# Kernel optimization log

Measured on AMD Instinct MI355X. Metric: run time of the kernel, lower is better.

## Reference

```python
import jax, jax.numpy as jnp
import numpy as np

SEQ_LEN, BATCH, IN_SIZE = 512, 1024, 3
HID, HID_FC, OUT = 512, 512, 1
HORIZON = 96


def gru_cell(x, h, w_ih, w_hh, b_ih, b_hh):
    # PyTorch GRU cell math. x: [B, in], h: [B, H], w_ih: [3H, in], w_hh: [3H, H]
    gi = x @ w_ih.T + b_ih
    gh = h @ w_hh.T + b_hh
    i_r, i_z, i_n = jnp.split(gi, 3, axis=-1)
    h_r, h_z, h_n = jnp.split(gh, 3, axis=-1)
    r = jax.nn.sigmoid(i_r + h_r)
    z = jax.nn.sigmoid(i_z + h_z)
    n = jnp.tanh(i_n + r * h_n)
    return (1.0 - z) * n + z * h


def setup_inputs() -> dict:
    key = jax.random.key(0)
    ks = jax.random.split(key, 16)
    s_in = 1.0 / np.sqrt(HID)
    inp = {
        'src': jax.random.normal(ks[0], (SEQ_LEN, BATCH, IN_SIZE), dtype=jnp.float32),
        'enc_wih': jax.random.uniform(ks[1], (3 * HID, IN_SIZE), minval=-s_in, maxval=s_in),
        'enc_whh': jax.random.uniform(ks[2], (3 * HID, HID), minval=-s_in, maxval=s_in),
        'enc_bih': jax.random.uniform(ks[3], (3 * HID,), minval=-s_in, maxval=s_in),
        'enc_bhh': jax.random.uniform(ks[4], (3 * HID,), minval=-s_in, maxval=s_in),
        'dec_wih': jax.random.uniform(ks[5], (3 * HID, OUT), minval=-s_in, maxval=s_in),
        'dec_whh': jax.random.uniform(ks[6], (3 * HID, HID), minval=-s_in, maxval=s_in),
        'dec_bih': jax.random.uniform(ks[7], (3 * HID,), minval=-s_in, maxval=s_in),
        'dec_bhh': jax.random.uniform(ks[8], (3 * HID,), minval=-s_in, maxval=s_in),
        'w1': jax.random.uniform(ks[9], (HID_FC, HID), minval=-s_in, maxval=s_in),
        'b1': jax.random.uniform(ks[10], (HID_FC,), minval=-s_in, maxval=s_in),
        'w2': jax.random.uniform(ks[11], (OUT, HID_FC), minval=-1.0 / np.sqrt(HID_FC), maxval=1.0 / np.sqrt(HID_FC)),
        'b2': jax.random.uniform(ks[12], (OUT,), minval=-1.0 / np.sqrt(HID_FC), maxval=1.0 / np.sqrt(HID_FC)),
        'horizon': HORIZON,
    }
    return inp


def reference(src, enc_wih, enc_whh, enc_bih, enc_bhh,
              dec_wih, dec_whh, dec_bih, dec_bhh,
              w1, b1, w2, b2, horizon):
    B = src.shape[1]
    h0 = jnp.zeros((B, HID), dtype=src.dtype)

    # Encoder: run GRU over time; only final hidden state is used.
    def enc_step(h, x_t):
        return gru_cell(x_t, h, enc_wih, enc_whh, enc_bih, enc_bhh), None
    h, _ = jax.lax.scan(enc_step, h0, src)

    dec_in0 = src[-1, :, 0:1]  # [B, 1]

    def dec_step(carry, _):
        dec_in, h = carry
        h = gru_cell(dec_in, h, dec_wih, dec_whh, dec_bih, dec_bhh)
        y = jax.nn.relu(h @ w1.T + b1) @ w2.T + b2  # [B, 1]
        return (y, h), y
    _, outputs = jax.lax.scan(dec_step, (dec_in0, h), None, length=horizon)
    return outputs  # [horizon, B, 1]
```

## Files before the change

kernel.cpp:

```cpp
#include <hip/hip_runtime.h>

typedef __bf16 bf16x8 __attribute__((ext_vector_type(8)));
typedef float f32x4 __attribute__((ext_vector_type(4)));

#define HID 512
#define BATCH 1024
#define SEQL 512
#define NWG 512
#define NTHR 256

#define OFF_ENH 0u
#define OFF_ENL 1572864u
#define OFF_DEH 3145728u
#define OFF_DEL 4718592u
#define OFF_W1H 6291456u
#define OFF_W1L 6815744u
#define OFF_HP0 7340032u
#define OFF_HP1 9437184u
#define OFF_FC1 11534336u
#define OFF_BAR 13631488u
#define WS_NEED 13639680u

#define LDS_LO 16384
#define SWZ(row, cb) (((row) << 10) + ((cb) ^ (((row) & 7) << 4)))

__device__ __forceinline__ f32x4 mfma16(bf16x8 a, bf16x8 b, f32x4 c) {
  return __builtin_amdgcn_mfma_f32_16x16x32_bf16(a, b, c, 0, 0, 0);
}
__device__ __forceinline__ float sig_(float x) { return 1.0f / (1.0f + __expf(-x)); }
__device__ __forceinline__ float tanh_(float x) { return 1.0f - 2.0f / (__expf(2.0f * x) + 1.0f); }

__device__ __forceinline__ unsigned long long ald64(const void* p) {
  return __hip_atomic_load((const unsigned long long*)p, __ATOMIC_RELAXED,
                           __HIP_MEMORY_SCOPE_AGENT);
}
__device__ __forceinline__ void ast32(void* p, unsigned v) {
  __hip_atomic_store((unsigned*)p, v, __ATOMIC_RELAXED, __HIP_MEMORY_SCOPE_AGENT);
}
__device__ __forceinline__ void astf(void* p, float v) {
  __hip_atomic_store((float*)p, v, __ATOMIC_RELAXED, __HIP_MEMORY_SCOPE_AGENT);
}

__global__ void split_w(const float* __restrict__ a, __bf16* __restrict__ hi,
                        __bf16* __restrict__ lo, int n) {
  int i = blockIdx.x * blockDim.x + threadIdx.x;
  if (i < n) {
    float v = a[i];
    __bf16 h = (__bf16)v;
    hi[i] = h;
    lo[i] = (__bf16)(v - (float)h);
  }
}

__device__ __forceinline__ void gbar(unsigned* cnt, unsigned target) {
  __syncthreads();
  if (threadIdx.x == 0) {
    __hip_atomic_fetch_add(cnt, 1u, __ATOMIC_RELAXED, __HIP_MEMORY_SCOPE_AGENT);
    int i = 0;
    while (__hip_atomic_load(cnt, __ATOMIC_RELAXED, __HIP_MEMORY_SCOPE_AGENT) < target) {
      __builtin_amdgcn_s_sleep(2);
      if (++i >= 30000) break;
    }
  }
  __syncthreads();
  __builtin_amdgcn_sched_barrier(0);
}

__device__ __forceinline__ void stage_h16(char* sm, const unsigned* hsrc, int row0, int tid) {
  const unsigned long long* src = (const unsigned long long*)hsrc + ((size_t)row0 << 8) + tid;
  unsigned long long b[16];
#pragma unroll
  for (int j = 0; j < 16; ++j) b[j] = ald64(src + (size_t)j * 256);
#pragma unroll
  for (int j = 0; j < 16; ++j) {
    const unsigned p0 = (unsigned)b[j];
    const unsigned p1 = (unsigned)(b[j] >> 32);
    const unsigned hw = (p0 & 0xffffu) | (p1 << 16);
    const unsigned lw = (p0 >> 16) | (p1 & 0xffff0000u);
    const int sa = SWZ(j, tid << 2);
    *(unsigned*)(sm + sa) = hw;
    *(unsigned*)(sm + LDS_LO + sa) = lw;
  }
}

__device__ __forceinline__ void gh3(const char* sm, int rl, int kbb,
                                    const __bf16* __restrict__ Bh,
                                    const __bf16* __restrict__ Bl,
                                    const int (&boff)[3], f32x4 (&acc)[3]) {
#pragma unroll 4
  for (int kc = 0; kc < 16; ++kc) {
    const int sa = SWZ(rl, (kc << 6) + kbb);
    bf16x8 ah = *(const bf16x8*)(sm + sa);
    bf16x8 al = *(const bf16x8*)(sm + LDS_LO + sa);
    const int ko = kc << 5;
#pragma unroll
    for (int f = 0; f < 3; ++f) {
      bf16x8 bh = *(const bf16x8*)(Bh + boff[f] + ko);
      bf16x8 bl = *(const bf16x8*)(Bl + boff[f] + ko);
      acc[f] = mfma16(ah, bh, acc[f]);
      acc[f] = mfma16(al, bh, acc[f]);
      acc[f] = mfma16(ah, bl, acc[f]);
    }
  }
}

__device__ __forceinline__ void gh1(const char* sm, int rl, int kbb,
                                    const __bf16* __restrict__ Bh,
                                    const __bf16* __restrict__ Bl, int boff, f32x4& acc) {
#pragma unroll 4
  for (int kc = 0; kc < 16; ++kc) {
    const int sa = SWZ(rl, (kc << 6) + kbb);
    bf16x8 ah = *(const bf16x8*)(sm + sa);
    bf16x8 al = *(const bf16x8*)(sm + LDS_LO + sa);
    const int ko = kc << 5;
    bf16x8 bh = *(const bf16x8*)(Bh + boff + ko);
    bf16x8 bl = *(const bf16x8*)(Bl + boff + ko);
    acc = mfma16(ah, bh, acc);
    acc = mfma16(al, bh, acc);
    acc = mfma16(ah, bl, acc);
  }
}

__global__ void __launch_bounds__(NTHR, 4) seq2seq_main(
    const float* __restrict__ src, const float* __restrict__ enc_wih,
    const float* __restrict__ enc_bih, const float* __restrict__ enc_bhh,
    const float* __restrict__ dec_wih, const float* __restrict__ dec_bih,
    const float* __restrict__ dec_bhh, const float* __restrict__ b1,
    const float* __restrict__ w2, const float* __restrict__ b2,
    const int* __restrict__ hor, float* __restrict__ out, char* __restrict__ ws) {
  __shared__ f32x4 smv[2048];
  char* sm = (char*)smv;
  float* yb = (float*)sm;

  const __bf16* ench_hi = (const __bf16*)(ws + OFF_ENH);
  const __bf16* ench_lo = (const __bf16*)(ws + OFF_ENL);
  const __bf16* dech_hi = (const __bf16*)(ws + OFF_DEH);
  const __bf16* dech_lo = (const __bf16*)(ws + OFF_DEL);
  const __bf16* w1h = (const __bf16*)(ws + OFF_W1H);
  const __bf16* w1l = (const __bf16*)(ws + OFF_W1L);
  unsigned* hp0 = (unsigned*)(ws + OFF_HP0);
  unsigned* hp1 = (unsigned*)(ws + OFF_HP1);
  float* fc1 = (float*)(ws + OFF_FC1);

  const int bid = blockIdx.x;
  const int G = bid >> 3;
  const int ct = bid & 7;
  const int tid = threadIdx.x;
  const int wv = tid >> 6;
  const int lane = tid & 63;
  const int lan15 = lane & 15;
  const int crow = (lane >> 4) << 2;
  const int kbe = (lane >> 4) << 3;
  const int kbb = kbe << 1;
  const int rl = lan15;
  const int row0 = G << 4;
  const int cg = (ct << 6) + (wv << 4) + lan15;

  unsigned* cnt = (unsigned*)(ws + OFF_BAR) + (G << 5);

  int boff[3];
#pragma unroll
  for (int g = 0; g < 3; ++g) boff[g] = ((g << 9) + cg) * HID + kbe;
  const int boff_fc = cg * HID + kbe;

  float wE[3][3], biE[3], bhE[3];
#pragma unroll
  for (int g = 0; g < 3; ++g) {
    const int j = (g << 9) + cg;
    wE[g][0] = enc_wih[j * 3 + 0];
    wE[g][1] = enc_wih[j * 3 + 1];
    wE[g][2] = enc_wih[j * 3 + 2];
    biE[g] = enc_bih[j];
    bhE[g] = enc_bhh[j];
  }

  const f32x4 zf = {0.0f, 0.0f, 0.0f, 0.0f};
  float hpv[4] = {0.f, 0.f, 0.f, 0.f};

  for (int t = 0; t < SEQL; ++t) {
    float xv[4][3];
#pragma unroll
    for (int reg = 0; reg < 4; ++reg) {
      const int row = row0 + crow + reg;
      const float* xp = src + ((size_t)t * BATCH + row) * 3;
      xv[reg][0] = xp[0];
      xv[reg][1] = xp[1];
      xv[reg][2] = xp[2];
    }

    f32x4 acc[3];
#pragma unroll
    for (int f = 0; f < 3; ++f) acc[f] = zf;

    if (t != 0) {
      stage_h16(sm, (t & 1) ? hp1 : hp0, row0, tid);
      __syncthreads();
      gh3(sm, rl, kbb, ench_hi, ench_lo, boff, acc);
    }

    unsigned* hn = ((t + 1) & 1) ? hp1 : hp0;
#pragma unroll
    for (int reg = 0; reg < 4; ++reg) {
      const int row = row0 + crow + reg;
      const float x0 = xv[reg][0], x1 = xv[reg][1], x2 = xv[reg][2];
      const float gir = fmaf(x0, wE[0][0], fmaf(x1, wE[0][1], fmaf(x2, wE[0][2], biE[0])));
      const float giz = fmaf(x0, wE[1][0], fmaf(x1, wE[1][1], fmaf(x2, wE[1][2], biE[1])));
      const float gin = fmaf(x0, wE[2][0], fmaf(x1, wE[2][1], fmaf(x2, wE[2][2], biE[2])));
      const float rg = sig_(gir + acc[0][reg] + bhE[0]);
      const float zg = sig_(giz + acc[1][reg] + bhE[1]);
      const float ng = tanh_(gin + rg * (acc[2][reg] + bhE[2]));
      const float hv = fmaf(zg, hpv[reg] - ng, ng);
      hpv[reg] = hv;
      const __bf16 hb = (__bf16)hv;
      const __bf16 lb = (__bf16)(hv - (float)hb);
      const unsigned pw = (unsigned)__builtin_bit_cast(unsigned short, hb) |
                          ((unsigned)__builtin_bit_cast(unsigned short, lb) << 16);
      ast32(hn + (size_t)row * HID + cg, pw);
    }
    gbar(cnt, 8u * (unsigned)(t + 1));
  }

  float wD[3], biD[3], bhD[3];
#pragma unroll
  for (int g = 0; g < 3; ++g) {
    const int j = (g << 9) + cg;
    wD[g] = dec_wih[j];
    biD[g] = dec_bih[j];
    bhD[g] = dec_bhh[j];
  }
  const float b1c = b1[cg];
  const float b2v = b2[0];
  float w2p0[4], w2p1[4];
#pragma unroll
  for (int j = 0; j < 4; ++j) {
    w2p0[j] = w2[2 * (lane + j * 64)];
    w2p1[j] = w2[2 * (lane + j * 64) + 1];
  }
  int H = hor[0];
  if (H < 1 || H > 96) H = 96;

  for (int t = 0; t < H; ++t) {
    float din[4];
    if (t == 0) {
#pragma unroll
      for (int reg = 0; reg < 4; ++reg) {
        const int row = row0 + crow + reg;
        din[reg] = src[((size_t)(SEQL - 1) * BATCH + row) * 3];
      }
    } else {
#pragma unroll
      for (int rr = 0; rr < 4; ++rr) {
        const int row = row0 + (wv << 2) + rr;
        const unsigned long long* fp = (const unsigned long long*)fc1 + ((size_t)row << 8);
        float s = 0.0f;
#pragma unroll
        for (int j = 0; j < 4; ++j) {
          const unsigned long long w = ald64(fp + lane + (j << 6));
          const float f0 = __builtin_bit_cast(float, (unsigned)(w & 0xffffffffULL));
          const float f1 = __builtin_bit_cast(float, (unsigned)(w >> 32));
          s = fmaf(f0, w2p0[j], fmaf(f1, w2p1[j], s));
        }
#pragma unroll
        for (int off = 1; off < 64; off <<= 1) s += __shfl_xor(s, off, 64);
        if (lane == 0) yb[(wv << 2) + rr] = s + b2v;
      }
      __syncthreads();
      if (ct == 0 && tid < 16) out[(size_t)(t - 1) * BATCH + row0 + tid] = yb[tid];
#pragma unroll
      for (int reg = 0; reg < 4; ++reg) din[reg] = yb[crow + reg];
      __syncthreads();
    }

    {
      stage_h16(sm, (t & 1) ? hp1 : hp0, row0, tid);
      __syncthreads();
      f32x4 acc[3];
#pragma unroll
      for (int f = 0; f < 3; ++f) acc[f] = zf;
      gh3(sm, rl, kbb, dech_hi, dech_lo, boff, acc);

      unsigned* hn = ((t + 1) & 1) ? hp1 : hp0;
#pragma unroll
      for (int reg = 0; reg < 4; ++reg) {
        const int row = row0 + crow + reg;
        const float d = din[reg];
        const float rg = sig_(fmaf(d, wD[0], biD[0]) + acc[0][reg] + bhD[0]);
        const float zg = sig_(fmaf(d, wD[1], biD[1]) + acc[1][reg] + bhD[1]);
        const float ng = tanh_(fmaf(d, wD[2], biD[2]) + rg * (acc[2][reg] + bhD[2]));
        const float hv = fmaf(zg, hpv[reg] - ng, ng);
        hpv[reg] = hv;
        const __bf16 hb = (__bf16)hv;
        const __bf16 lb = (__bf16)(hv - (float)hb);
        const unsigned pw = (unsigned)__builtin_bit_cast(unsigned short, hb) |
                            ((unsigned)__builtin_bit_cast(unsigned short, lb) << 16);
        ast32(hn + (size_t)row * HID + cg, pw);
      }
    }
    gbar(cnt, 8u * (unsigned)(SEQL + 2 * t + 1));

    {
      stage_h16(sm, ((t + 1) & 1) ? hp1 : hp0, row0, tid);
      __syncthreads();
      f32x4 fa = zf;
      gh1(sm, rl, kbb, w1h, w1l, boff_fc, fa);
#pragma unroll
      for (int reg = 0; reg < 4; ++reg) {
        const int row = row0 + crow + reg;
        astf(&fc1[(size_t)row * HID + cg], fmaxf(fa[reg] + b1c, 0.0f));
      }
    }
    gbar(cnt, 8u * (unsigned)(SEQL + 2 * t + 2));
  }

  if (ct == 0) {
#pragma unroll
    for (int rr = 0; rr < 4; ++rr) {
      const int row = row0 + (wv << 2) + rr;
      const unsigned long long* fp = (const unsigned long long*)fc1 + ((size_t)row << 8);
      float s = 0.0f;
#pragma unroll
      for (int j = 0; j < 4; ++j) {
        const unsigned long long w = ald64(fp + lane + (j << 6));
        const float f0 = __builtin_bit_cast(float, (unsigned)(w & 0xffffffffULL));
        const float f1 = __builtin_bit_cast(float, (unsigned)(w >> 32));
        s = fmaf(f0, w2p0[j], fmaf(f1, w2p1[j], s));
      }
#pragma unroll
      for (int off = 1; off < 64; off <<= 1) s += __shfl_xor(s, off, 64);
      if (lane == 0) yb[(wv << 2) + rr] = s + b2v;
    }
    __syncthreads();
    if (tid < 16) out[(size_t)(H - 1) * BATCH + row0 + tid] = yb[tid];
  }
}

extern "C" void kernel_launch(void* const* d_in, const int* in_sizes, int n_in,
                              void* d_out, int out_size, void* d_ws, size_t ws_size,
                              hipStream_t stream) {
  if (ws_size < WS_NEED) return;

  const float* src = (const float*)d_in[0];
  const float* enc_wih = (const float*)d_in[1];
  const float* enc_whh = (const float*)d_in[2];
  const float* enc_bih = (const float*)d_in[3];
  const float* enc_bhh = (const float*)d_in[4];
  const float* dec_wih = (const float*)d_in[5];
  const float* dec_whh = (const float*)d_in[6];
  const float* dec_bih = (const float*)d_in[7];
  const float* dec_bhh = (const float*)d_in[8];
  const float* w1 = (const float*)d_in[9];
  const float* b1 = (const float*)d_in[10];
  const float* w2 = (const float*)d_in[11];
  const float* b2 = (const float*)d_in[12];
  const int* hor = (const int*)d_in[13];
  float* out = (float*)d_out;
  char* ws = (char*)d_ws;

  hipMemsetAsync(ws + OFF_BAR, 0, 8192, stream);

  split_w<<<dim3(3072), dim3(256), 0, stream>>>(enc_whh, (__bf16*)(ws + OFF_ENH),
                                                (__bf16*)(ws + OFF_ENL), 786432);
  split_w<<<dim3(3072), dim3(256), 0, stream>>>(dec_whh, (__bf16*)(ws + OFF_DEH),
                                                (__bf16*)(ws + OFF_DEL), 786432);
  split_w<<<dim3(1024), dim3(256), 0, stream>>>(w1, (__bf16*)(ws + OFF_W1H),
                                                (__bf16*)(ws + OFF_W1L), 262144);

  seq2seq_main<<<dim3(NWG), dim3(NTHR), 0, stream>>>(
      src, enc_wih, enc_bih, enc_bhh, dec_wih, dec_bih, dec_bhh, b1, w2, b2, hor, out, ws);
}
```

Baseline: 15.33 ms.

## Give each workgroup a full batch tile and keep hidden state in LDS

The work split changes from 512 workgroups (8 column tiles per 16-row batch group, tied together by global-memory barriers) to 64 workgroups of 512 threads. Each workgroup now owns all 512 hidden columns for its 16 batch rows. Hidden state stays in LDS, so the global h exchange, the atomic spin barriers and the fc1 round trip through memory go away, and the FC2 reduction is done in LDS. The trade-off is that only 64 workgroups run on a GPU with many more CUs, and each one streams the full recurrent weights from cache every step, so far less of the chip is used.

New measurement: 55.52 ms. +262.3%, slower.

```diff
diff --git a/kernel.cpp b/kernel.cpp
--- a/kernel.cpp
+++ b/kernel.cpp
@@ -2,12 +2,13 @@
 
 typedef __bf16 bf16x8 __attribute__((ext_vector_type(8)));
 typedef float f32x4 __attribute__((ext_vector_type(4)));
+typedef unsigned u32x4 __attribute__((ext_vector_type(4)));
 
 #define HID 512
 #define BATCH 1024
 #define SEQL 512
-#define NWG 512
-#define NTHR 256
+#define NWG 64
+#define NTHR 512
 
 #define OFF_ENH 0u
 #define OFF_ENL 1572864u
@@ -15,31 +16,17 @@
 #define OFF_DEL 4718592u
 #define OFF_W1H 6291456u
 #define OFF_W1L 6815744u
-#define OFF_HP0 7340032u
-#define OFF_HP1 9437184u
-#define OFF_FC1 11534336u
-#define OFF_BAR 13631488u
-#define WS_NEED 13639680u
-
-#define LDS_LO 16384
-#define SWZ(row, cb) (((row) << 10) + ((cb) ^ (((row) & 7) << 4)))
+#define WS_NEED 7340032u
+
+#define LDS_PS 32768
+#define LDS_Y 33280
+#define SWZP(row, cb) (((row) << 11) + ((cb) ^ (((row) & 7) << 4)))
 
 __device__ __forceinline__ f32x4 mfma16(bf16x8 a, bf16x8 b, f32x4 c) {
   return __builtin_amdgcn_mfma_f32_16x16x32_bf16(a, b, c, 0, 0, 0);
 }
 __device__ __forceinline__ float sig_(float x) { return 1.0f / (1.0f + __expf(-x)); }
 __device__ __forceinline__ float tanh_(float x) { return 1.0f - 2.0f / (__expf(2.0f * x) + 1.0f); }
-
-__device__ __forceinline__ unsigned long long ald64(const void* p) {
-  return __hip_atomic_load((const unsigned long long*)p, __ATOMIC_RELAXED,
-                           __HIP_MEMORY_SCOPE_AGENT);
-}
-__device__ __forceinline__ void ast32(void* p, unsigned v) {
-  __hip_atomic_store((unsigned*)p, v, __ATOMIC_RELAXED, __HIP_MEMORY_SCOPE_AGENT);
-}
-__device__ __forceinline__ void astf(void* p, float v) {
-  __hip_atomic_store((float*)p, v, __ATOMIC_RELAXED, __HIP_MEMORY_SCOPE_AGENT);
-}
 
 __global__ void split_w(const float* __restrict__ a, __bf16* __restrict__ hi,
                         __bf16* __restrict__ lo, int n) {
@@ -52,85 +39,34 @@
   }
 }
 
-__device__ __forceinline__ void gbar(unsigned* cnt, unsigned target) {
-  __syncthreads();
-  if (threadIdx.x == 0) {
-    __hip_atomic_fetch_add(cnt, 1u, __ATOMIC_RELAXED, __HIP_MEMORY_SCOPE_AGENT);
-    int i = 0;
-    while (__hip_atomic_load(cnt, __ATOMIC_RELAXED, __HIP_MEMORY_SCOPE_AGENT) < target) {
-      __builtin_amdgcn_s_sleep(2);
-      if (++i >= 30000) break;
-    }
-  }
-  __syncthreads();
-  __builtin_amdgcn_sched_barrier(0);
-}
-
-__device__ __forceinline__ void stage_h16(char* sm, const unsigned* hsrc, int row0, int tid) {
-  const unsigned long long* src = (const unsigned long long*)hsrc + ((size_t)row0 << 8) + tid;
-  unsigned long long b[16];
-#pragma unroll
-  for (int j = 0; j < 16; ++j) b[j] = ald64(src + (size_t)j * 256);
-#pragma unroll
-  for (int j = 0; j < 16; ++j) {
-    const unsigned p0 = (unsigned)b[j];
-    const unsigned p1 = (unsigned)(b[j] >> 32);
-    const unsigned hw = (p0 & 0xffffu) | (p1 << 16);
-    const unsigned lw = (p0 >> 16) | (p1 & 0xffff0000u);
-    const int sa = SWZ(j, tid << 2);
-    *(unsigned*)(sm + sa) = hw;
-    *(unsigned*)(sm + LDS_LO + sa) = lw;
-  }
-}
-
-__device__ __forceinline__ void gh3(const char* sm, int rl, int kbb,
-                                    const __bf16* __restrict__ Bh,
-                                    const __bf16* __restrict__ Bl,
-                                    const int (&boff)[3], f32x4 (&acc)[3]) {
-#pragma unroll 4
-  for (int kc = 0; kc < 16; ++kc) {
-    const int sa = SWZ(rl, (kc << 6) + kbb);
-    bf16x8 ah = *(const bf16x8*)(sm + sa);
-    bf16x8 al = *(const bf16x8*)(sm + LDS_LO + sa);
-    const int ko = kc << 5;
-#pragma unroll
-    for (int f = 0; f < 3; ++f) {
-      bf16x8 bh = *(const bf16x8*)(Bh + boff[f] + ko);
-      bf16x8 bl = *(const bf16x8*)(Bl + boff[f] + ko);
-      acc[f] = mfma16(ah, bh, acc[f]);
-      acc[f] = mfma16(al, bh, acc[f]);
-      acc[f] = mfma16(ah, bl, acc[f]);
-    }
-  }
-}
-
-__device__ __forceinline__ void gh1(const char* sm, int rl, int kbb,
-                                    const __bf16* __restrict__ Bh,
-                                    const __bf16* __restrict__ Bl, int boff, f32x4& acc) {
-#pragma unroll 4
-  for (int kc = 0; kc < 16; ++kc) {
-    const int sa = SWZ(rl, (kc << 6) + kbb);
-    bf16x8 ah = *(const bf16x8*)(sm + sa);
-    bf16x8 al = *(const bf16x8*)(sm + LDS_LO + sa);
-    const int ko = kc << 5;
-    bf16x8 bh = *(const bf16x8*)(Bh + boff + ko);
-    bf16x8 bl = *(const bf16x8*)(Bl + boff + ko);
-    acc = mfma16(ah, bh, acc);
-    acc = mfma16(al, bh, acc);
-    acc = mfma16(ah, bl, acc);
-  }
-}
-
-__global__ void __launch_bounds__(NTHR, 4) seq2seq_main(
+__device__ __forceinline__ void rd_afrag(const char* sm, int lan15, int cb, bf16x8& ah,
+                                         bf16x8& al) {
+  const u32x4 q0 = *(const u32x4*)(sm + SWZP(lan15, cb));
+  const u32x4 q1 = *(const u32x4*)(sm + SWZP(lan15, cb + 16));
+  u32x4 h, l;
+  h.x = (q0.x & 0xffffu) | (q0.y << 16);
+  h.y = (q0.z & 0xffffu) | (q0.w << 16);
+  h.z = (q1.x & 0xffffu) | (q1.y << 16);
+  h.w = (q1.z & 0xffffu) | (q1.w << 16);
+  l.x = (q0.x >> 16) | (q0.y & 0xffff0000u);
+  l.y = (q0.z >> 16) | (q0.w & 0xffff0000u);
+  l.z = (q1.x >> 16) | (q1.y & 0xffff0000u);
+  l.w = (q1.z >> 16) | (q1.w & 0xffff0000u);
+  ah = __builtin_bit_cast(bf16x8, h);
+  al = __builtin_bit_cast(bf16x8, l);
+}
+
+__global__ void __launch_bounds__(NTHR, 2) seq2seq_main(
     const float* __restrict__ src, const float* __restrict__ enc_wih,
     const float* __restrict__ enc_bih, const float* __restrict__ enc_bhh,
     const float* __restrict__ dec_wih, const float* __restrict__ dec_bih,
     const float* __restrict__ dec_bhh, const float* __restrict__ b1,
     const float* __restrict__ w2, const float* __restrict__ b2,
     const int* __restrict__ hor, float* __restrict__ out, char* __restrict__ ws) {
-  __shared__ f32x4 smv[2048];
+  __shared__ f32x4 smv[2084];
   char* sm = (char*)smv;
-  float* yb = (float*)sm;
+  float* psum = (float*)(sm + LDS_PS);
+  float* ylds = (float*)(sm + LDS_Y);
 
   const __bf16* ench_hi = (const __bf16*)(ws + OFF_ENH);
   const __bf16* ench_lo = (const __bf16*)(ws + OFF_ENL);
@@ -138,199 +74,256 @@
   const __bf16* dech_lo = (const __bf16*)(ws + OFF_DEL);
   const __bf16* w1h = (const __bf16*)(ws + OFF_W1H);
   const __bf16* w1l = (const __bf16*)(ws + OFF_W1L);
-  unsigned* hp0 = (unsigned*)(ws + OFF_HP0);
-  unsigned* hp1 = (unsigned*)(ws + OFF_HP1);
-  float* fc1 = (float*)(ws + OFF_FC1);
-
-  const int bid = blockIdx.x;
-  const int G = bid >> 3;
-  const int ct = bid & 7;
+
+  const int G = blockIdx.x;
+  const int row0 = G << 4;
   const int tid = threadIdx.x;
   const int wv = tid >> 6;
   const int lane = tid & 63;
   const int lan15 = lane & 15;
-  const int crow = (lane >> 4) << 2;
-  const int kbe = (lane >> 4) << 3;
-  const int kbb = kbe << 1;
-  const int rl = lan15;
-  const int row0 = G << 4;
-  const int cg = (ct << 6) + (wv << 4) + lan15;
-
-  unsigned* cnt = (unsigned*)(ws + OFF_BAR) + (G << 5);
-
-  int boff[3];
-#pragma unroll
-  for (int g = 0; g < 3; ++g) boff[g] = ((g << 9) + cg) * HID + kbe;
-  const int boff_fc = cg * HID + kbe;
-
-  float wE[3][3], biE[3], bhE[3];
-#pragma unroll
-  for (int g = 0; g < 3; ++g) {
-    const int j = (g << 9) + cg;
-    wE[g][0] = enc_wih[j * 3 + 0];
-    wE[g][1] = enc_wih[j * 3 + 1];
-    wE[g][2] = enc_wih[j * 3 + 2];
-    biE[g] = enc_bih[j];
-    bhE[g] = enc_bhh[j];
-  }
+  const int l4 = lane >> 4;
+  const int kbe = l4 << 3;
+
+  int boff[3][4];
+#pragma unroll
+  for (int g = 0; g < 3; ++g)
+#pragma unroll
+    for (int nf = 0; nf < 4; ++nf)
+      boff[g][nf] = (((g << 9) + (wv << 6) + (nf << 4) + lan15) << 9) + kbe;
+  int bofffc[4];
+#pragma unroll
+  for (int nf = 0; nf < 4; ++nf) bofffc[nf] = (((wv << 6) + (nf << 4) + lan15) << 9) + kbe;
+
+  float wE[3][4][3], biE[3][4], bhE[3][4];
+#pragma unroll
+  for (int g = 0; g < 3; ++g)
+#pragma unroll
+    for (int nf = 0; nf < 4; ++nf) {
+      const int j = (g << 9) + (wv << 6) + (nf << 4) + lan15;
+      wE[g][nf][0] = enc_wih[j * 3 + 0];
+      wE[g][nf][1] = enc_wih[j * 3 + 1];
+      wE[g][nf][2] = enc_wih[j * 3 + 2];
+      biE[g][nf] = enc_bih[j];
+      bhE[g][nf] = enc_bhh[j];
+    }
 
   const f32x4 zf = {0.0f, 0.0f, 0.0f, 0.0f};
-  float hpv[4] = {0.f, 0.f, 0.f, 0.f};
+  float hpv[4][4];
+#pragma unroll
+  for (int nf = 0; nf < 4; ++nf)
+#pragma unroll
+    for (int reg = 0; reg < 4; ++reg) hpv[nf][reg] = 0.0f;
 
   for (int t = 0; t < SEQL; ++t) {
     float xv[4][3];
 #pragma unroll
     for (int reg = 0; reg < 4; ++reg) {
-      const int row = row0 + crow + reg;
-      const float* xp = src + ((size_t)t * BATCH + row) * 3;
+      const int grow = row0 + (l4 << 2) + reg;
+      const float* xp = src + ((size_t)t * BATCH + grow) * 3;
       xv[reg][0] = xp[0];
       xv[reg][1] = xp[1];
       xv[reg][2] = xp[2];
     }
 
-    f32x4 acc[3];
-#pragma unroll
-    for (int f = 0; f < 3; ++f) acc[f] = zf;
+    f32x4 acc[3][4];
+#pragma unroll
+    for (int g = 0; g < 3; ++g)
+#pragma unroll
+      for (int nf = 0; nf < 4; ++nf) acc[g][nf] = zf;
 
     if (t != 0) {
-      stage_h16(sm, (t & 1) ? hp1 : hp0, row0, tid);
-      __syncthreads();
-      gh3(sm, rl, kbb, ench_hi, ench_lo, boff, acc);
-    }
-
-    unsigned* hn = ((t + 1) & 1) ? hp1 : hp0;
+#pragma unroll 4
+      for (int kc = 0; kc < 16; ++kc) {
+        bf16x8 ah, al;
+        rd_afrag(sm, lan15, (kc << 7) + (l4 << 5), ah, al);
+        const int ko = kc << 5;
+#pragma unroll
+        for (int g = 0; g < 3; ++g)
+#pragma unroll
+          for (int nf = 0; nf < 4; ++nf) {
+            bf16x8 bh = *(const bf16x8*)(ench_hi + boff[g][nf] + ko);
+            bf16x8 bl = *(const bf16x8*)(ench_lo + boff[g][nf] + ko);
+            acc[g][nf] = mfma16(ah, bh, acc[g][nf]);
+            acc[g][nf] = mfma16(al, bh, acc[g][nf]);
+            acc[g][nf] = mfma16(ah, bl, acc[g][nf]);
+          }
+      }
+    }
+    __syncthreads();
+
 #pragma unroll
     for (int reg = 0; reg < 4; ++reg) {
-      const int row = row0 + crow + reg;
+      const int row = (l4 << 2) + reg;
       const float x0 = xv[reg][0], x1 = xv[reg][1], x2 = xv[reg][2];
-      const float gir = fmaf(x0, wE[0][0], fmaf(x1, wE[0][1], fmaf(x2, wE[0][2], biE[0])));
-      const float giz = fmaf(x0, wE[1][0], fmaf(x1, wE[1][1], fmaf(x2, wE[1][2], biE[1])));
-      const float gin = fmaf(x0, wE[2][0], fmaf(x1, wE[2][1], fmaf(x2, wE[2][2], biE[2])));
-      const float rg = sig_(gir + acc[0][reg] + bhE[0]);
-      const float zg = sig_(giz + acc[1][reg] + bhE[1]);
-      const float ng = tanh_(gin + rg * (acc[2][reg] + bhE[2]));
-      const float hv = fmaf(zg, hpv[reg] - ng, ng);
-      hpv[reg] = hv;
-      const __bf16 hb = (__bf16)hv;
-      const __bf16 lb = (__bf16)(hv - (float)hb);
-      const unsigned pw = (unsigned)__builtin_bit_cast(unsigned short, hb) |
-                          ((unsigned)__builtin_bit_cast(unsigned short, lb) << 16);
-      ast32(hn + (size_t)row * HID + cg, pw);
-    }
-    gbar(cnt, 8u * (unsigned)(t + 1));
-  }
-
-  float wD[3], biD[3], bhD[3];
-#pragma unroll
-  for (int g = 0; g < 3; ++g) {
-    const int j = (g << 9) + cg;
-    wD[g] = dec_wih[j];
-    biD[g] = dec_bih[j];
-    bhD[g] = dec_bhh[j];
-  }
-  const float b1c = b1[cg];
-  const float b2v = b2[0];
-  float w2p0[4], w2p1[4];
-#pragma unroll
-  for (int j = 0; j < 4; ++j) {
-    w2p0[j] = w2[2 * (lane + j * 64)];
-    w2p1[j] = w2[2 * (lane + j * 64) + 1];
-  }
-  int H = hor[0];
-  if (H < 1 || H > 96) H = 96;
-
-  for (int t = 0; t < H; ++t) {
-    float din[4];
-    if (t == 0) {
-#pragma unroll
-      for (int reg = 0; reg < 4; ++reg) {
-        const int row = row0 + crow + reg;
-        din[reg] = src[((size_t)(SEQL - 1) * BATCH + row) * 3];
-      }
-    } else {
-#pragma unroll
-      for (int rr = 0; rr < 4; ++rr) {
-        const int row = row0 + (wv << 2) + rr;
-        const unsigned long long* fp = (const unsigned long long*)fc1 + ((size_t)row << 8);
-        float s = 0.0f;
-#pragma unroll
-        for (int j = 0; j < 4; ++j) {
-          const unsigned long long w = ald64(fp + lane + (j << 6));
-          const float f0 = __builtin_bit_cast(float, (unsigned)(w & 0xffffffffULL));
-          const float f1 = __builtin_bit_cast(float, (unsigned)(w >> 32));
-          s = fmaf(f0, w2p0[j], fmaf(f1, w2p1[j], s));
-        }
-#pragma unroll
-        for (int off = 1; off < 64; off <<= 1) s += __shfl_xor(s, off, 64);
-        if (lane == 0) yb[(wv << 2) + rr] = s + b2v;
-      }
-      __syncthreads();
-      if (ct == 0 && tid < 16) out[(size_t)(t - 1) * BATCH + row0 + tid] = yb[tid];
-#pragma unroll
-      for (int reg = 0; reg < 4; ++reg) din[reg] = yb[crow + reg];
-      __syncthreads();
-    }
-
-    {
-      stage_h16(sm, (t & 1) ? hp1 : hp0, row0, tid);
-      __syncthreads();
-      f32x4 acc[3];
-#pragma unroll
-      for (int f = 0; f < 3; ++f) acc[f] = zf;
-      gh3(sm, rl, kbb, dech_hi, dech_lo, boff, acc);
-
-      unsigned* hn = ((t + 1) & 1) ? hp1 : hp0;
-#pragma unroll
-      for (int reg = 0; reg < 4; ++reg) {
-        const int row = row0 + crow + reg;
-        const float d = din[reg];
-        const float rg = sig_(fmaf(d, wD[0], biD[0]) + acc[0][reg] + bhD[0]);
-        const float zg = sig_(fmaf(d, wD[1], biD[1]) + acc[1][reg] + bhD[1]);
-        const float ng = tanh_(fmaf(d, wD[2], biD[2]) + rg * (acc[2][reg] + bhD[2]));
-        const float hv = fmaf(zg, hpv[reg] - ng, ng);
-        hpv[reg] = hv;
+#pragma unroll
+      for (int nf = 0; nf < 4; ++nf) {
+        const float gir =
+            fmaf(x0, wE[0][nf][0], fmaf(x1, wE[0][nf][1], fmaf(x2, wE[0][nf][2], biE[0][nf])));
+        const float giz =
+            fmaf(x0, wE[1][nf][0], fmaf(x1, wE[1][nf][1], fmaf(x2, wE[1][nf][2], biE[1][nf])));
+        const float gin =
+            fmaf(x0, wE[2][nf][0], fmaf(x1, wE[2][nf][1], fmaf(x2, wE[2][nf][2], biE[2][nf])));
+        const float rg = sig_(gir + acc[0][nf][reg] + bhE[0][nf]);
+        const float zg = sig_(giz + acc[1][nf][reg] + bhE[1][nf]);
+        const float ng = tanh_(gin + rg * (acc[2][nf][reg] + bhE[2][nf]));
+        const float hv = fmaf(zg, hpv[nf][reg] - ng, ng);
+        hpv[nf][reg] = hv;
         const __bf16 hb = (__bf16)hv;
         const __bf16 lb = (__bf16)(hv - (float)hb);
         const unsigned pw = (unsigned)__builtin_bit_cast(unsigned short, hb) |
                             ((unsigned)__builtin_bit_cast(unsigned short, lb) << 16);
-        ast32(hn + (size_t)row * HID + cg, pw);
-      }
-    }
-    gbar(cnt, 8u * (unsigned)(SEQL + 2 * t + 1));
-
-    {
-      stage_h16(sm, ((t + 1) & 1) ? hp1 : hp0, row0, tid);
+        const int col = (wv << 6) + (nf << 4) + lan15;
+        *(unsigned*)(sm + SWZP(row, col << 2)) = pw;
+      }
+    }
+    __syncthreads();
+  }
+
+  float wD[3][4], biD[3][4], bhD[3][4], b1c[4], w2v[4];
+#pragma unroll
+  for (int g = 0; g < 3; ++g)
+#pragma unroll
+    for (int nf = 0; nf < 4; ++nf) {
+      const int j = (g << 9) + (wv << 6) + (nf << 4) + lan15;
+      wD[g][nf] = dec_wih[j];
+      biD[g][nf] = dec_bih[j];
+      bhD[g][nf] = dec_bhh[j];
+    }
+#pragma unroll
+  for (int nf = 0; nf < 4; ++nf) {
+    const int fcol = (wv << 6) + (nf << 4) + lan15;
+    b1c[nf] = b1[fcol];
+    w2v[nf] = w2[fcol];
+  }
+  const float b2v = b2[0];
+  int H = hor[0];
+  if (H < 1 || H > 96) H = 96;
+
+  float facc[4][4];
+
+  for (int t = 0; t < H; ++t) {
+    float din[4];
+    if (t == 0) {
+#pragma unroll
+      for (int reg = 0; reg < 4; ++reg)
+        din[reg] = src[((size_t)(SEQL - 1) * BATCH + row0 + (l4 << 2) + reg) * 3];
+    } else {
+      float ps[4];
+#pragma unroll
+      for (int reg = 0; reg < 4; ++reg) {
+        ps[reg] = facc[0][reg] * w2v[0];
+#pragma unroll
+        for (int nf = 1; nf < 4; ++nf) ps[reg] = fmaf(facc[nf][reg], w2v[nf], ps[reg]);
+#pragma unroll
+        for (int off = 1; off < 16; off <<= 1) ps[reg] += __shfl_xor(ps[reg], off, 64);
+      }
+      if (lan15 == 0) {
+#pragma unroll
+        for (int reg = 0; reg < 4; ++reg) psum[(((l4 << 2) + reg) << 3) + wv] = ps[reg];
+      }
       __syncthreads();
-      f32x4 fa = zf;
-      gh1(sm, rl, kbb, w1h, w1l, boff_fc, fa);
-#pragma unroll
-      for (int reg = 0; reg < 4; ++reg) {
-        const int row = row0 + crow + reg;
-        astf(&fc1[(size_t)row * HID + cg], fmaxf(fa[reg] + b1c, 0.0f));
-      }
-    }
-    gbar(cnt, 8u * (unsigned)(SEQL + 2 * t + 2));
-  }
-
-  if (ct == 0) {
-#pragma unroll
-    for (int rr = 0; rr < 4; ++rr) {
-      const int row = row0 + (wv << 2) + rr;
-      const unsigned long long* fp = (const unsigned long long*)fc1 + ((size_t)row << 8);
-      float s = 0.0f;
-#pragma unroll
-      for (int j = 0; j < 4; ++j) {
-        const unsigned long long w = ald64(fp + lane + (j << 6));
-        const float f0 = __builtin_bit_cast(float, (unsigned)(w & 0xffffffffULL));
-        const float f1 = __builtin_bit_cast(float, (unsigned)(w >> 32));
-        s = fmaf(f0, w2p0[j], fmaf(f1, w2p1[j], s));
-      }
-#pragma unroll
-      for (int off = 1; off < 64; off <<= 1) s += __shfl_xor(s, off, 64);
-      if (lane == 0) yb[(wv << 2) + rr] = s + b2v;
-    }
-    __syncthreads();
-    if (tid < 16) out[(size_t)(H - 1) * BATCH + row0 + tid] = yb[tid];
+      if (wv == 0 && lane < 16) {
+        float s = b2v;
+#pragma unroll
+        for (int j = 0; j < 8; ++j) s += psum[(lane << 3) + j];
+        ylds[lane] = s;
+        out[(size_t)(t - 1) * BATCH + row0 + lane] = s;
+      }
+      __syncthreads();
+#pragma unroll
+      for (int reg = 0; reg < 4; ++reg) din[reg] = ylds[(l4 << 2) + reg];
+    }
+
+    f32x4 acc[3][4];
+#pragma unroll
+    for (int g = 0; g < 3; ++g)
+#pragma unroll
+      for (int nf = 0; nf < 4; ++nf) acc[g][nf] = zf;
+#pragma unroll 4
+    for (int kc = 0; kc < 16; ++kc) {
+      bf16x8 ah, al;
+      rd_afrag(sm, lan15, (kc << 7) + (l4 << 5), ah, al);
+      const int ko = kc << 5;
+#pragma unroll
+      for (int g = 0; g < 3; ++g)
+#pragma unroll
+        for (int nf = 0; nf < 4; ++nf) {
+          bf16x8 bh = *(const bf16x8*)(dech_hi + boff[g][nf] + ko);
+          bf16x8 bl = *(const bf16x8*)(dech_lo + boff[g][nf] + ko);
+          acc[g][nf] = mfma16(ah, bh, acc[g][nf]);
+          acc[g][nf] = mfma16(al, bh, acc[g][nf]);
+          acc[g][nf] = mfma16(ah, bl, acc[g][nf]);
+        }
+    }
+    __syncthreads();
+
+#pragma unroll
+    for (int reg = 0; reg < 4; ++reg) {
+      const int row = (l4 << 2) + reg;
+      const float d = din[reg];
+#pragma unroll
+      for (int nf = 0; nf < 4; ++nf) {
+        const float rg = sig_(fmaf(d, wD[0][nf], biD[0][nf]) + acc[0][nf][reg] + bhD[0][nf]);
+        const float zg = sig_(fmaf(d, wD[1][nf], biD[1][nf]) + acc[1][nf][reg] + bhD[1][nf]);
+        const float ng =
+            tanh_(fmaf(d, wD[2][nf], biD[2][nf]) + rg * (acc[2][nf][reg] + bhD[2][nf]));
+        const float hv = fmaf(zg, hpv[nf][reg] - ng, ng);
+        hpv[nf][reg] = hv;
+        const __bf16 hb = (__bf16)hv;
+        const __bf16 lb = (__bf16)(hv - (float)hb);
+        const unsigned pw = (unsigned)__builtin_bit_cast(unsigned short, hb) |
+                            ((unsigned)__builtin_bit_cast(unsigned short, lb) << 16);
+        const int col = (wv << 6) + (nf << 4) + lan15;
+        *(unsigned*)(sm + SWZP(row, col << 2)) = pw;
+      }
+    }
+    __syncthreads();
+
+    f32x4 fa[4];
+#pragma unroll
+    for (int nf = 0; nf < 4; ++nf) fa[nf] = zf;
+#pragma unroll 4
+    for (int kc = 0; kc < 16; ++kc) {
+      bf16x8 ah, al;
+      rd_afrag(sm, lan15, (kc << 7) + (l4 << 5), ah, al);
+      const int ko = kc << 5;
+#pragma unroll
+      for (int nf = 0; nf < 4; ++nf) {
+        bf16x8 bh = *(const bf16x8*)(w1h + bofffc[nf] + ko);
+        bf16x8 bl = *(const bf16x8*)(w1l + bofffc[nf] + ko);
+        fa[nf] = mfma16(ah, bh, fa[nf]);
+        fa[nf] = mfma16(al, bh, fa[nf]);
+        fa[nf] = mfma16(ah, bl, fa[nf]);
+      }
+    }
+#pragma unroll
+    for (int nf = 0; nf < 4; ++nf)
+#pragma unroll
+      for (int reg = 0; reg < 4; ++reg) facc[nf][reg] = fmaxf(fa[nf][reg] + b1c[nf], 0.0f);
+  }
+
+  {
+    float ps[4];
+#pragma unroll
+    for (int reg = 0; reg < 4; ++reg) {
+      ps[reg] = facc[0][reg] * w2v[0];
+#pragma unroll
+      for (int nf = 1; nf < 4; ++nf) ps[reg] = fmaf(facc[nf][reg], w2v[nf], ps[reg]);
+#pragma unroll
+      for (int off = 1; off < 16; off <<= 1) ps[reg] += __shfl_xor(ps[reg], off, 64);
+    }
+    __syncthreads();
+    if (lan15 == 0) {
+#pragma unroll
+      for (int reg = 0; reg < 4; ++reg) psum[(((l4 << 2) + reg) << 3) + wv] = ps[reg];
+    }
+    __syncthreads();
+    if (wv == 0 && lane < 16) {
+      float s = b2v;
+#pragma unroll
+      for (int j = 0; j < 8; ++j) s += psum[(lane << 3) + j];
+      out[(size_t)(H - 1) * BATCH + row0 + lane] = s;
+    }
   }
 }
 
@@ -356,8 +349,6 @@
   float* out = (float*)d_out;
   char* ws = (char*)d_ws;
 
-  hipMemsetAsync(ws + OFF_BAR, 0, 8192, stream);
-
   split_w<<<dim3(3072), dim3(256), 0, stream>>>(enc_whh, (__bf16*)(ws + OFF_ENH),
                                                 (__bf16*)(ws + OFF_ENL), 786432);
   split_w<<<dim3(3072), dim3(256), 0, stream>>>(dec_whh, (__bf16*)(ws + OFF_DEH),
```
